# Kernel optimization log

Measured on AMD Instinct MI355X. Metric: run time of the kernel, lower is better.

## Reference

```python
import jax, jax.numpy as jnp
import numpy as np

N_HEAD = 8
D_HEAD = 64
D_MODEL = 512
CTX = 64
B = 2
Q_LEN = 2048
T = Q_LEN + CTX - 1


def setup_inputs() -> dict:
    key = jax.random.key(0)
    ks = jax.random.split(key, 7)
    HD = N_HEAD * D_HEAD
    return {
        "x": jax.random.normal(ks[0], (B, T, D_MODEL), jnp.float32),
        "r": jax.random.normal(ks[1], (CTX, D_MODEL), jnp.float32),
        "Wkv": jax.random.normal(ks[2], (D_MODEL, 2 * HD), jnp.float32) * 0.02,
        "Wq": jax.random.normal(ks[3], (D_MODEL, HD), jnp.float32) * 0.02,
        "bq": jax.random.normal(ks[4], (HD,), jnp.float32) * 0.02,
        "Wr": jax.random.normal(ks[5], (D_MODEL, HD), jnp.float32) * 0.02,
        "Wo": jax.random.normal(ks[6], (HD, D_MODEL), jnp.float32) * 0.02,
    }


def reference(x, r, Wkv, Wq, bq, Wr, Wo):
    Bb, Tt, _ = x.shape
    C = r.shape[0]
    H, Dh = N_HEAD, D_HEAD
    q_len = Tt - C + 1
    scale = Dh ** -0.5

    kv = x @ Wkv                                  # [B, T, 2*H*Dh]
    k_all = kv[..., : H * Dh].reshape(Bb, Tt, H, Dh)
    v_all = kv[..., H * Dh:].reshape(Bb, Tt, H, Dh)

    # sliding windows (torch unfold(1, ctx, 1) equivalent)
    idx = jnp.arange(q_len)[:, None] + jnp.arange(C)[None, :]   # [q, C]
    k_win = k_all[:, idx]                         # [B, q, C, H, Dh]
    v_win = v_all[:, idx]                         # [B, q, C, H, Dh]

    hq = (x[:, C - 1:] @ Wq + bq).reshape(Bb, q_len, H, Dh)     # [B, q, H, Dh]
    hr = (r @ Wr).reshape(C, H, Dh)                              # [C, H, Dh]

    # q . (k + r): split into content term + relative-position bias term
    scores = (jnp.einsum('bqhd,bqchd->bhqc', hq, k_win)
              + jnp.einsum('bqhd,chd->bhqc', hq, hr)) * scale    # [B, H, q, C]

    # padding mask: positions in first ctx-1 steps that are all-zero
    pad_mask = jnp.all(x[:, : C - 1] == 0, axis=-1)              # [B, C-1]
    full_mask = jnp.concatenate(
        [pad_mask, jnp.zeros((Bb, q_len), dtype=bool)], axis=1)  # [B, T]
    mask_win = full_mask[:, idx]                                 # [B, q, C]
    scores = jnp.where(mask_win[:, None], -jnp.inf, scores)

    w = jax.nn.softmax(scores, axis=-1)                          # [B, H, q, C]
    out = jnp.einsum('bhqc,bqchd->bqhd', w, v_win).reshape(Bb, q_len, H * Dh)
    return out @ Wo                                              # [B, q, d_model]
```

## Files before the change

kernel.cpp:

```cpp
#include <hip/hip_runtime.h>
#include <cstdint>
#include <cstddef>

#define NH 8
#define DH 64
#define DM 512
#define CTX 64
#define BB 2
#define QL 2048
#define TT (QL + CTX - 1)
#define HDIM 512
#define KVN 1024
#define KD 512

typedef unsigned short u16;
typedef __attribute__((ext_vector_type(8))) short bf16x8;
typedef __attribute__((ext_vector_type(4))) float f32x4;

__device__ __forceinline__ u16 f2bf(float f) {
    uint32_t u = __float_as_uint(f);
    u += 0x7FFF + ((u >> 16) & 1);
    return (u16)(u >> 16);
}
__device__ __forceinline__ uint32_t packbf(float lo, float hi) {
    return (uint32_t)f2bf(lo) | ((uint32_t)f2bf(hi) << 16);
}

#define GLLDS(g, l) __builtin_amdgcn_global_load_lds( \
    (const __attribute__((address_space(1))) void*)(g), \
    (__attribute__((address_space(3))) void*)(l), 16, 0, 0)

__global__ __launch_bounds__(256) void prep_kernel(
    const float* __restrict__ Wkv, const float* __restrict__ Wq,
    const float* __restrict__ Wr, const float* __restrict__ Wo,
    u16* __restrict__ WkvqT, u16* __restrict__ WrT, u16* __restrict__ WoT)
{
    __shared__ float tile[64][65];
    const int bid = blockIdx.x;
    const int tid = threadIdx.x;

    const float* W; u16* WT; int N; int tidx;
    if (bid < 128)      { W = Wkv; WT = WkvqT;                    N = 1024; tidx = bid; }
    else if (bid < 192) { W = Wq;  WT = WkvqT + (size_t)1024*512; N = 512;  tidx = bid - 128; }
    else if (bid < 256) { W = Wr;  WT = WrT;                      N = 512;  tidx = bid - 192; }
    else                { W = Wo;  WT = WoT;                      N = 512;  tidx = bid - 256; }
    const int tpr = N / 64;
    const int kb = (tidx / tpr) * 64, nb = (tidx % tpr) * 64;
    const int c4 = (tid & 15) * 4;
    for (int kk = tid >> 4; kk < 64; kk += 16) {
        float4 v = *(const float4*)&W[(size_t)(kb + kk) * N + nb + c4];
        tile[kk][c4 + 0] = v.x; tile[kk][c4 + 1] = v.y;
        tile[kk][c4 + 2] = v.z; tile[kk][c4 + 3] = v.w;
    }
    __syncthreads();
    for (int nn = tid >> 4; nn < 64; nn += 16) {
        ushort4 o;
        o.x = f2bf(tile[c4 + 0][nn]); o.y = f2bf(tile[c4 + 1][nn]);
        o.z = f2bf(tile[c4 + 2][nn]); o.w = f2bf(tile[c4 + 3][nn]);
        *(ushort4*)&WT[(size_t)(nb + nn) * KD + kb + c4] = o;
    }
}

__global__ __launch_bounds__(256) void gemm_fused(
    const float* __restrict__ x, const u16* __restrict__ WkvqT,
    u16* __restrict__ kvb, u16* __restrict__ hqb, const float* __restrict__ bq,
    const float* __restrict__ r, const u16* __restrict__ WrT,
    u16* __restrict__ hrb, float* __restrict__ maskv)
{
    const int bid = blockIdx.x;
    const int tid = threadIdx.x;

    if (bid >= 400) {
        __shared__ int anyflag;
        int idx = bid - 400;
        int t = idx >> 1, b = idx & 1;
        const float* row = x + (size_t)(b * TT + t) * DM;
        bool nz = (row[tid] != 0.f) || (row[tid + 256] != 0.f);
        if (tid == 0) anyflag = 0;
        __syncthreads();
        unsigned long long bal = __ballot(nz);
        if ((tid & 63) == 0 && bal) atomicOr(&anyflag, 1);
        __syncthreads();
        if (tid == 0) maskv[b * 64 + t] = anyflag ? 0.f : -1e30f;
        return;
    }

    __shared__ __align__(16) u16 As[2][128 * 32];
    __shared__ __align__(16) u16 Bs[2][128 * 32];

    const int lane = tid & 63;
    const int w    = tid >> 6;
    const int wm   = (w >> 1) * 64;
    const int wn   = (w & 1) * 64;

    const bool g3 = (bid >= 396);
    const float* A; const u16* BT; int m0, n0, mrows;
    if (g3) { A = r; BT = WrT;   m0 = 0;                n0 = (bid - 396) * 128; mrows = CTX; }
    else    { A = x; BT = WkvqT; m0 = (bid / 12) * 128; n0 = (bid % 12) * 128;  mrows = BB * TT; }

    const int arow = tid >> 1;
    const int akh  = (tid & 1) * 16;
    int grow = m0 + arow; if (grow >= mrows) grow = 0;
    const float* gA = A + (size_t)grow * KD + akh;

    const int am0 = tid >> 2;
    const int ak0 = (tid & 3) * 8;
    const u16* gb0 = BT + (size_t)(n0 + am0) * KD + ak0;
    const u16* gb1 = gb0 + (size_t)64 * KD;

    float4 f0, f1, f2, f3;
#define ALOAD(kt) do { \
    f0 = *(const float4*)(gA + (kt));      f1 = *(const float4*)(gA + (kt) + 4); \
    f2 = *(const float4*)(gA + (kt) + 8);  f3 = *(const float4*)(gA + (kt) + 12); \
} while (0)
#define AWRITE(buf) do { \
    uint4 p0, p1; \
    p0.x = packbf(f0.x, f0.y); p0.y = packbf(f0.z, f0.w); \
    p0.z = packbf(f1.x, f1.y); p0.w = packbf(f1.z, f1.w); \
    p1.x = packbf(f2.x, f2.y); p1.y = packbf(f2.z, f2.w); \
    p1.z = packbf(f3.x, f3.y); p1.w = packbf(f3.z, f3.w); \
    *(uint4*)&As[buf][arow * 32 + akh]     = p0; \
    *(uint4*)&As[buf][arow * 32 + akh + 8] = p1; \
} while (0)
#define BSTAGE(buf, kt) do { \
    GLLDS(gb0 + (kt), &Bs[buf][(size_t)w * 512]); \
    GLLDS(gb1 + (kt), &Bs[buf][2048 + (size_t)w * 512]); \
} while (0)

    f32x4 acc[4][4];
#pragma unroll
    for (int i = 0; i < 4; i++)
#pragma unroll
        for (int j = 0; j < 4; j++)
            acc[i][j] = (f32x4){0.f, 0.f, 0.f, 0.f};

    ALOAD(0);
    AWRITE(0);
    BSTAGE(0, 0);
    __syncthreads();

    int cur = 0;
    const int fm = lane & 15;
    const int fk = (lane >> 4) * 8;
    for (int kt = 0; kt < KD; kt += 32) {
        const bool more = (kt + 32 < KD);
        if (more) { ALOAD(kt + 32); BSTAGE(cur ^ 1, kt + 32); }

        bf16x8 af[4], bfr[4];
#pragma unroll
        for (int i = 0; i < 4; i++)
            af[i] = *(const bf16x8*)&As[cur][(wm + i * 16 + fm) * 32 + fk];
#pragma unroll
        for (int j = 0; j < 4; j++)
            bfr[j] = *(const bf16x8*)&Bs[cur][(wn + j * 16 + fm) * 32 + fk];
#pragma unroll
        for (int i = 0; i < 4; i++)
#pragma unroll
            for (int j = 0; j < 4; j++)
                acc[i][j] = __builtin_amdgcn_mfma_f32_16x16x32_bf16(af[i], bfr[j], acc[i][j], 0, 0, 0);

        if (more) AWRITE(cur ^ 1);
        __syncthreads();
        cur ^= 1;
    }
#undef ALOAD
#undef AWRITE
#undef BSTAGE

    const int fc = lane & 15;
    const int fr = (lane >> 4) * 4;
    if (!g3) {
        const bool iskv = (n0 < 1024);
#pragma unroll
        for (int i = 0; i < 4; i++)
#pragma unroll
            for (int rr = 0; rr < 4; rr++) {
                int row = m0 + wm + i * 16 + fr + rr;
                if (row < BB * TT) {
                    if (iskv) {
#pragma unroll
                        for (int j = 0; j < 4; j++) {
                            int col = n0 + wn + j * 16 + fc;
                            kvb[(size_t)row * KVN + col] = f2bf(acc[i][j][rr]);
                        }
                    } else {
                        int bb = row / TT;
                        int t  = row - bb * TT;
                        if (t >= CTX - 1) {
                            size_t orow = (size_t)(bb * QL + t - (CTX - 1));
#pragma unroll
                            for (int j = 0; j < 4; j++) {
                                int col = n0 + wn + j * 16 + fc - 1024;
                                hqb[orow * HDIM + col] = f2bf(acc[i][j][rr] + bq[col]);
                            }
                        }
                    }
                }
            }
    } else {
#pragma unroll
        for (int i = 0; i < 4; i++)
#pragma unroll
            for (int rr = 0; rr < 4; rr++) {
                int row = m0 + wm + i * 16 + fr + rr;
                if (row < CTX) {
#pragma unroll
                    for (int j = 0; j < 4; j++) {
                        int col = n0 + wn + j * 16 + fc;
                        hrb[(size_t)row * HDIM + col] = f2bf(acc[i][j][rr]);
                    }
                }
            }
    }
}

__global__ __launch_bounds__(256) void gemm_n64(
    const u16* __restrict__ A, const u16* __restrict__ BT,
    float* __restrict__ C, int M, int N)
{
    __shared__ u16 As[2][128 * 32];
    __shared__ u16 Bs[2][64 * 32];

    const int tid  = threadIdx.x;
    const int lane = tid & 63;
    const int w    = tid >> 6;
    const int wm   = (w >> 1) * 64;
    const int wn   = (w & 1) * 32;
    const int m0   = blockIdx.y * 128;
    const int n0   = blockIdx.x * 64;

    const int am0 = tid >> 2;
    const int ak0 = (tid & 3) * 8;
    const u16* ga0 = A  + (size_t)(m0 + am0) * KD + ak0;
    const u16* ga1 = ga0 + (size_t)64 * KD;
    const u16* gb0 = BT + (size_t)(n0 + am0) * KD + ak0;

#define STAGE_G2(buf, kt) do { \
    GLLDS(ga0 + (kt), &As[buf][(size_t)w * 512]); \
    GLLDS(ga1 + (kt), &As[buf][2048 + (size_t)w * 512]); \
    GLLDS(gb0 + (kt), &Bs[buf][(size_t)w * 512]); \
} while (0)

    f32x4 acc[4][2];
#pragma unroll
    for (int i = 0; i < 4; i++)
#pragma unroll
        for (int j = 0; j < 2; j++)
            acc[i][j] = (f32x4){0.f, 0.f, 0.f, 0.f};

    STAGE_G2(0, 0);
    __syncthreads();

    int cur = 0;
    const int fm = lane & 15;
    const int fk = (lane >> 4) * 8;
    for (int kt = 0; kt < KD; kt += 32) {
        if (kt + 32 < KD) STAGE_G2(cur ^ 1, kt + 32);

        bf16x8 af[4], bfr[2];
#pragma unroll
        for (int i = 0; i < 4; i++)
            af[i] = *(const bf16x8*)&As[cur][(wm + i * 16 + fm) * 32 + fk];
#pragma unroll
        for (int j = 0; j < 2; j++)
            bfr[j] = *(const bf16x8*)&Bs[cur][(wn + j * 16 + fm) * 32 + fk];
#pragma unroll
        for (int i = 0; i < 4; i++)
#pragma unroll
            for (int j = 0; j < 2; j++)
                acc[i][j] = __builtin_amdgcn_mfma_f32_16x16x32_bf16(af[i], bfr[j], acc[i][j], 0, 0, 0);

        __syncthreads();
        cur ^= 1;
    }
#undef STAGE_G2

    const int fc = lane & 15;
    const int fr = (lane >> 4) * 4;
#pragma unroll
    for (int i = 0; i < 4; i++)
#pragma unroll
        for (int rr = 0; rr < 4; rr++) {
            int row = m0 + wm + i * 16 + fr + rr;
            if (row < M) {
#pragma unroll
                for (int j = 0; j < 2; j++) {
                    int col = n0 + wn + j * 16 + fc;
                    C[(size_t)row * N + col] = acc[i][j][rr];
                }
            }
        }
}

__global__ __launch_bounds__(256) void attn_mfma(
    const u16* __restrict__ kvb, const u16* __restrict__ hqb,
    const u16* __restrict__ hrb, const float* __restrict__ maskv,
    u16* __restrict__ attnb)
{
    __shared__ __align__(16) char lds[55296];
    float* sprime = (float*)lds;
    u16*   vTs    = (u16*)(lds + 20480);
    u16*   wband  = (u16*)(lds + 37888);

    const int q0 = blockIdx.x * 64;
    const int h  = blockIdx.y;
    const int b  = blockIdx.z;
    const int tid  = threadIdx.x;
    const int lane = tid & 63;
    const int w    = tid >> 6;
    const int qb   = q0 + w * 16;

    const int vr0 = tid >> 4;
    const int vc4 = (tid & 15) * 4;
    ushort4 vreg[8];
#pragma unroll
    for (int i = 0; i < 8; i++) {
        int rr = vr0 + i * 16;
        if (rr < 127)
            vreg[i] = *(const ushort4*)&kvb[(size_t)(b * TT + q0 + rr) * KVN + HDIM + h * DH + vc4];
        else
            vreg[i] = (ushort4){0, 0, 0, 0};
    }

    {
        uint32_t* wz = (uint32_t*)wband;
#pragma unroll
        for (int i = 0; i < 17; i++) wz[tid + i * 256] = 0;
    }
    asm volatile("s_waitcnt lgkmcnt(0)" ::: "memory");
    __builtin_amdgcn_s_barrier();

    const int fm = lane & 15;
    const int fk = (lane >> 4) * 8;

    const u16* hqrow = hqb + (size_t)(b * QL + qb + fm) * HDIM + h * DH + fk;
    bf16x8 afr0 = *(const bf16x8*)(hqrow);
    bf16x8 afr1 = *(const bf16x8*)(hqrow + 32);

    {
        const u16* kbase = kvb + (size_t)(b * TT + qb + fm) * KVN + h * DH + fk;
#pragma unroll
        for (int nt = 0; nt < 5; nt++) {
            bf16x8 b0 = *(const bf16x8*)(kbase + (size_t)nt * 16 * KVN);
            bf16x8 b1 = *(const bf16x8*)(kbase + (size_t)nt * 16 * KVN + 32);
            f32x4 acc = (f32x4){0.f, 0.f, 0.f, 0.f};
            acc = __builtin_amdgcn_mfma_f32_16x16x32_bf16(afr0, b0, acc, 0, 0, 0);
            acc = __builtin_amdgcn_mfma_f32_16x16x32_bf16(afr1, b1, acc, 0, 0, 0);
            const int row = (lane >> 4) * 4;
#pragma unroll
            for (int r = 0; r < 4; r++)
                sprime[w * 1280 + (row + r) * 80 + nt * 16 + fm] = acc[r];
        }
    }
    {
        const u16* hrbase = hrb + (size_t)fm * HDIM + h * DH + fk;
#pragma unroll
        for (int nc = 0; nc < 4; nc++) {
            bf16x8 b0 = *(const bf16x8*)(hrbase + (size_t)nc * 16 * HDIM);
            bf16x8 b1 = *(const bf16x8*)(hrbase + (size_t)nc * 16 * HDIM + 32);
            f32x4 acc = (f32x4){0.f, 0.f, 0.f, 0.f};
            acc = __builtin_amdgcn_mfma_f32_16x16x32_bf16(afr0, b0, acc, 0, 0, 0);
            acc = __builtin_amdgcn_mfma_f32_16x16x32_bf16(afr1, b1, acc, 0, 0, 0);
            const int row = (lane >> 4) * 4;
#pragma unroll
            for (int r = 0; r < 4; r++)
                sprime[w * 1280 + (row + r) * 81 + nc * 16 + fm] += acc[r];
        }
    }

#pragma unroll
    for (int i = 0; i < 8; i++) {
        int rr = vr0 + i * 16;
        vTs[(vc4 + 0) * 136 + rr] = vreg[i].x;
        vTs[(vc4 + 1) * 136 + rr] = vreg[i].y;
        vTs[(vc4 + 2) * 136 + rr] = vreg[i].z;
        vTs[(vc4 + 3) * 136 + rr] = vreg[i].w;
    }

    {
        const int i  = lane >> 2;
        const int g  = lane & 3;
        const int qloc = w * 16 + i;
        const float* srow = &sprime[w * 1280 + i * 81 + g * 16];
        float sv[16];
#pragma unroll
        for (int j = 0; j < 16; j++) sv[j] = srow[j] * 0.125f;
        if (q0 == 0) {
#pragma unroll
            for (int j = 0; j < 16; j++) {
                int t = qloc + g * 16 + j;
                if (t < 63) sv[j] += maskv[b * 64 + t];
            }
        }
        float mx = sv[0];
#pragma unroll
        for (int j = 1; j < 16; j++) mx = fmaxf(mx, sv[j]);
        mx = fmaxf(mx, __shfl_xor(mx, 1, 64));
        mx = fmaxf(mx, __shfl_xor(mx, 2, 64));
        float sum = 0.f;
#pragma unroll
        for (int j = 0; j < 16; j++) { sv[j] = __expf(sv[j] - mx); sum += sv[j]; }
        sum += __shfl_xor(sum, 1, 64);
        sum += __shfl_xor(sum, 2, 64);
        float inv = 1.f / sum;
        u16* wrow = &wband[qloc * 136 + qloc + g * 16];
#pragma unroll
        for (int j = 0; j < 16; j++) wrow[j] = f2bf(sv[j] * inv);
    }
    __syncthreads();

    f32x4 oacc[4];
#pragma unroll
    for (int j = 0; j < 4; j++) oacc[j] = (f32x4){0.f, 0.f, 0.f, 0.f};
#pragma unroll
    for (int ks = 0; ks < 4; ks++) {
        bf16x8 wa = *(const bf16x8*)&wband[(w * 16 + fm) * 136 + ks * 32 + fk];
#pragma unroll
        for (int j = 0; j < 4; j++) {
            bf16x8 vb = *(const bf16x8*)&vTs[(j * 16 + fm) * 136 + ks * 32 + fk];
            oacc[j] = __builtin_amdgcn_mfma_f32_16x16x32_bf16(wa, vb, oacc[j], 0, 0, 0);
        }
    }
    {
        const int row = (lane >> 4) * 4;
#pragma unroll
        for (int j = 0; j < 4; j++)
#pragma unroll
            for (int r = 0; r < 4; r++)
                attnb[(size_t)(b * QL + qb + row + r) * HDIM + h * DH + j * 16 + fm] =
                    f2bf(oacc[j][r]);
    }
}

extern "C" void kernel_launch(void* const* d_in, const int* in_sizes, int n_in,
                              void* d_out, int out_size, void* d_ws, size_t ws_size,
                              hipStream_t stream)
{
    const float* x   = (const float*)d_in[0];
    const float* r   = (const float*)d_in[1];
    const float* Wkv = (const float*)d_in[2];
    const float* Wq  = (const float*)d_in[3];
    const float* bq  = (const float*)d_in[4];
    const float* Wr  = (const float*)d_in[5];
    const float* Wo  = (const float*)d_in[6];
    float* out = (float*)d_out;

    char* p = (char*)d_ws;
    u16* WkvqT  = (u16*)p;  p += (size_t)1536 * 512 * 2;
    u16* WrT    = (u16*)p;  p += (size_t)512 * 512 * 2;
    u16* WoT    = (u16*)p;  p += (size_t)512 * 512 * 2;
    u16* kvb    = (u16*)p;  p += (size_t)4224 * 1024 * 2;
    u16* hqb    = (u16*)p;  p += (size_t)4096 * 512 * 2;
    u16* hrb    = (u16*)p;  p += (size_t)64 * 512 * 2;
    u16* attnb  = (u16*)p;  p += (size_t)4096 * 512 * 2;
    float* maskv = (float*)p;

    hipLaunchKernelGGL(prep_kernel, dim3(320), dim3(256), 0, stream,
                       Wkv, Wq, Wr, Wo, WkvqT, WrT, WoT);
    hipLaunchKernelGGL(gemm_fused, dim3(528), dim3(256), 0, stream,
                       x, WkvqT, kvb, hqb, bq, r, WrT, hrb, maskv);
    hipLaunchKernelGGL(attn_mfma, dim3(QL / 64, NH, BB), dim3(256), 0, stream,
                       kvb, hqb, hrb, maskv, attnb);
    hipLaunchKernelGGL(gemm_n64, dim3(512 / 64, 4096 / 128), dim3(256), 0, stream,
                       attnb, WoT, out, 4096, 512);
}
```

Before: 125.4 us.

## Fuse all stages into one cooperative persistent kernel with grid syncs

Merges the weight-prep, QKV/R projection GEMM, attention and output GEMM kernels into a single cooperative kernel of 512 blocks that separates the stages with grid.sync, falling back to four separate launches if the cooperative launch fails. The mask computation moves from the projection GEMM into the prep stage. The output GEMM is retiled from 128x64 to 64x64 so its 512 tiles match the grid. The aim is to remove per-launch overhead and inter-kernel gaps. In exchange, the kernel carries the 55 KB LDS footprint of the attention stage everywhere, and the stages pay grid-barrier costs and run many idle blocks.

```diff
diff --git a/kernel.cpp b/kernel.cpp
--- a/kernel.cpp
+++ b/kernel.cpp
@@ -1,6 +1,9 @@
 #include <hip/hip_runtime.h>
+#include <hip/hip_cooperative_groups.h>
 #include <cstdint>
 #include <cstddef>
+
+namespace cg = cooperative_groups;
 
 #define NH 8
 #define DH 64
@@ -30,63 +33,60 @@
     (const __attribute__((address_space(1))) void*)(g), \
     (__attribute__((address_space(3))) void*)(l), 16, 0, 0)
 
-__global__ __launch_bounds__(256) void prep_kernel(
+__device__ __forceinline__ void st_prep(
+    char* lds, int bid, int tid,
+    const float* __restrict__ x,
     const float* __restrict__ Wkv, const float* __restrict__ Wq,
     const float* __restrict__ Wr, const float* __restrict__ Wo,
-    u16* __restrict__ WkvqT, u16* __restrict__ WrT, u16* __restrict__ WoT)
-{
-    __shared__ float tile[64][65];
-    const int bid = blockIdx.x;
-    const int tid = threadIdx.x;
-
-    const float* W; u16* WT; int N; int tidx;
-    if (bid < 128)      { W = Wkv; WT = WkvqT;                    N = 1024; tidx = bid; }
-    else if (bid < 192) { W = Wq;  WT = WkvqT + (size_t)1024*512; N = 512;  tidx = bid - 128; }
-    else if (bid < 256) { W = Wr;  WT = WrT;                      N = 512;  tidx = bid - 192; }
-    else                { W = Wo;  WT = WoT;                      N = 512;  tidx = bid - 256; }
-    const int tpr = N / 64;
-    const int kb = (tidx / tpr) * 64, nb = (tidx % tpr) * 64;
-    const int c4 = (tid & 15) * 4;
-    for (int kk = tid >> 4; kk < 64; kk += 16) {
-        float4 v = *(const float4*)&W[(size_t)(kb + kk) * N + nb + c4];
-        tile[kk][c4 + 0] = v.x; tile[kk][c4 + 1] = v.y;
-        tile[kk][c4 + 2] = v.z; tile[kk][c4 + 3] = v.w;
-    }
-    __syncthreads();
-    for (int nn = tid >> 4; nn < 64; nn += 16) {
-        ushort4 o;
-        o.x = f2bf(tile[c4 + 0][nn]); o.y = f2bf(tile[c4 + 1][nn]);
-        o.z = f2bf(tile[c4 + 2][nn]); o.w = f2bf(tile[c4 + 3][nn]);
-        *(ushort4*)&WT[(size_t)(nb + nn) * KD + kb + c4] = o;
-    }
-}
-
-__global__ __launch_bounds__(256) void gemm_fused(
+    u16* __restrict__ WkvqT, u16* __restrict__ WrT, u16* __restrict__ WoT,
+    float* __restrict__ maskv)
+{
+    if (bid < 320) {
+        float (*tile)[65] = (float (*)[65])lds;
+        const float* W; u16* WT; int N; int tidx;
+        if (bid < 128)      { W = Wkv; WT = WkvqT;                    N = 1024; tidx = bid; }
+        else if (bid < 192) { W = Wq;  WT = WkvqT + (size_t)1024*512; N = 512;  tidx = bid - 128; }
+        else if (bid < 256) { W = Wr;  WT = WrT;                      N = 512;  tidx = bid - 192; }
+        else                { W = Wo;  WT = WoT;                      N = 512;  tidx = bid - 256; }
+        const int tpr = N / 64;
+        const int kb = (tidx / tpr) * 64, nb = (tidx % tpr) * 64;
+        const int c4 = (tid & 15) * 4;
+        for (int kk = tid >> 4; kk < 64; kk += 16) {
+            float4 v = *(const float4*)&W[(size_t)(kb + kk) * N + nb + c4];
+            tile[kk][c4 + 0] = v.x; tile[kk][c4 + 1] = v.y;
+            tile[kk][c4 + 2] = v.z; tile[kk][c4 + 3] = v.w;
+        }
+        __syncthreads();
+        for (int nn = tid >> 4; nn < 64; nn += 16) {
+            ushort4 o;
+            o.x = f2bf(tile[c4 + 0][nn]); o.y = f2bf(tile[c4 + 1][nn]);
+            o.z = f2bf(tile[c4 + 2][nn]); o.w = f2bf(tile[c4 + 3][nn]);
+            *(ushort4*)&WT[(size_t)(nb + nn) * KD + kb + c4] = o;
+        }
+    } else {
+        int* anyflag = (int*)lds;
+        int idx = bid - 320;
+        int t = idx >> 1, b = idx & 1;
+        const float* row = x + (size_t)(b * TT + t) * DM;
+        bool nz = (row[tid] != 0.f) || (row[tid + 256] != 0.f);
+        if (tid == 0) *anyflag = 0;
+        __syncthreads();
+        unsigned long long bal = __ballot(nz);
+        if ((tid & 63) == 0 && bal) atomicOr(anyflag, 1);
+        __syncthreads();
+        if (tid == 0) maskv[b * 64 + t] = *anyflag ? 0.f : -1e30f;
+    }
+}
+
+__device__ __forceinline__ void st_g1(
+    char* lds, int bid, int tid,
     const float* __restrict__ x, const u16* __restrict__ WkvqT,
     u16* __restrict__ kvb, u16* __restrict__ hqb, const float* __restrict__ bq,
     const float* __restrict__ r, const u16* __restrict__ WrT,
-    u16* __restrict__ hrb, float* __restrict__ maskv)
-{
-    const int bid = blockIdx.x;
-    const int tid = threadIdx.x;
-
-    if (bid >= 400) {
-        __shared__ int anyflag;
-        int idx = bid - 400;
-        int t = idx >> 1, b = idx & 1;
-        const float* row = x + (size_t)(b * TT + t) * DM;
-        bool nz = (row[tid] != 0.f) || (row[tid + 256] != 0.f);
-        if (tid == 0) anyflag = 0;
-        __syncthreads();
-        unsigned long long bal = __ballot(nz);
-        if ((tid & 63) == 0 && bal) atomicOr(&anyflag, 1);
-        __syncthreads();
-        if (tid == 0) maskv[b * 64 + t] = anyflag ? 0.f : -1e30f;
-        return;
-    }
-
-    __shared__ __align__(16) u16 As[2][128 * 32];
-    __shared__ __align__(16) u16 Bs[2][128 * 32];
+    u16* __restrict__ hrb)
+{
+    u16 (*As)[128 * 32] = (u16 (*)[128 * 32])lds;
+    u16 (*Bs)[128 * 32] = (u16 (*)[128 * 32])(lds + 16384);
 
     const int lane = tid & 63;
     const int w    = tid >> 6;
@@ -109,11 +109,11 @@
     const u16* gb1 = gb0 + (size_t)64 * KD;
 
     float4 f0, f1, f2, f3;
-#define ALOAD(kt) do { \
+#define ALOAD1(kt) do { \
     f0 = *(const float4*)(gA + (kt));      f1 = *(const float4*)(gA + (kt) + 4); \
     f2 = *(const float4*)(gA + (kt) + 8);  f3 = *(const float4*)(gA + (kt) + 12); \
 } while (0)
-#define AWRITE(buf) do { \
+#define AWRITE1(buf) do { \
     uint4 p0, p1; \
     p0.x = packbf(f0.x, f0.y); p0.y = packbf(f0.z, f0.w); \
     p0.z = packbf(f1.x, f1.y); p0.w = packbf(f1.z, f1.w); \
@@ -122,7 +122,7 @@
     *(uint4*)&As[buf][arow * 32 + akh]     = p0; \
     *(uint4*)&As[buf][arow * 32 + akh + 8] = p1; \
 } while (0)
-#define BSTAGE(buf, kt) do { \
+#define BSTAGE1(buf, kt) do { \
     GLLDS(gb0 + (kt), &Bs[buf][(size_t)w * 512]); \
     GLLDS(gb1 + (kt), &Bs[buf][2048 + (size_t)w * 512]); \
 } while (0)
@@ -134,9 +134,9 @@
         for (int j = 0; j < 4; j++)
             acc[i][j] = (f32x4){0.f, 0.f, 0.f, 0.f};
 
-    ALOAD(0);
-    AWRITE(0);
-    BSTAGE(0, 0);
+    ALOAD1(0);
+    AWRITE1(0);
+    BSTAGE1(0, 0);
     __syncthreads();
 
     int cur = 0;
@@ -144,7 +144,7 @@
     const int fk = (lane >> 4) * 8;
     for (int kt = 0; kt < KD; kt += 32) {
         const bool more = (kt + 32 < KD);
-        if (more) { ALOAD(kt + 32); BSTAGE(cur ^ 1, kt + 32); }
+        if (more) { ALOAD1(kt + 32); BSTAGE1(cur ^ 1, kt + 32); }
 
         bf16x8 af[4], bfr[4];
 #pragma unroll
@@ -159,13 +159,13 @@
             for (int j = 0; j < 4; j++)
                 acc[i][j] = __builtin_amdgcn_mfma_f32_16x16x32_bf16(af[i], bfr[j], acc[i][j], 0, 0, 0);
 
-        if (more) AWRITE(cur ^ 1);
+        if (more) AWRITE1(cur ^ 1);
         __syncthreads();
         cur ^= 1;
     }
-#undef ALOAD
-#undef AWRITE
-#undef BSTAGE
+#undef ALOAD1
+#undef AWRITE1
+#undef BSTAGE1
 
     const int fc = lane & 15;
     const int fr = (lane >> 4) * 4;
@@ -214,98 +214,19 @@
     }
 }
 
-__global__ __launch_bounds__(256) void gemm_n64(
-    const u16* __restrict__ A, const u16* __restrict__ BT,
-    float* __restrict__ C, int M, int N)
-{
-    __shared__ u16 As[2][128 * 32];
-    __shared__ u16 Bs[2][64 * 32];
-
-    const int tid  = threadIdx.x;
-    const int lane = tid & 63;
-    const int w    = tid >> 6;
-    const int wm   = (w >> 1) * 64;
-    const int wn   = (w & 1) * 32;
-    const int m0   = blockIdx.y * 128;
-    const int n0   = blockIdx.x * 64;
-
-    const int am0 = tid >> 2;
-    const int ak0 = (tid & 3) * 8;
-    const u16* ga0 = A  + (size_t)(m0 + am0) * KD + ak0;
-    const u16* ga1 = ga0 + (size_t)64 * KD;
-    const u16* gb0 = BT + (size_t)(n0 + am0) * KD + ak0;
-
-#define STAGE_G2(buf, kt) do { \
-    GLLDS(ga0 + (kt), &As[buf][(size_t)w * 512]); \
-    GLLDS(ga1 + (kt), &As[buf][2048 + (size_t)w * 512]); \
-    GLLDS(gb0 + (kt), &Bs[buf][(size_t)w * 512]); \
-} while (0)
-
-    f32x4 acc[4][2];
-#pragma unroll
-    for (int i = 0; i < 4; i++)
-#pragma unroll
-        for (int j = 0; j < 2; j++)
-            acc[i][j] = (f32x4){0.f, 0.f, 0.f, 0.f};
-
-    STAGE_G2(0, 0);
-    __syncthreads();
-
-    int cur = 0;
-    const int fm = lane & 15;
-    const int fk = (lane >> 4) * 8;
-    for (int kt = 0; kt < KD; kt += 32) {
-        if (kt + 32 < KD) STAGE_G2(cur ^ 1, kt + 32);
-
-        bf16x8 af[4], bfr[2];
-#pragma unroll
-        for (int i = 0; i < 4; i++)
-            af[i] = *(const bf16x8*)&As[cur][(wm + i * 16 + fm) * 32 + fk];
-#pragma unroll
-        for (int j = 0; j < 2; j++)
-            bfr[j] = *(const bf16x8*)&Bs[cur][(wn + j * 16 + fm) * 32 + fk];
-#pragma unroll
-        for (int i = 0; i < 4; i++)
-#pragma unroll
-            for (int j = 0; j < 2; j++)
-                acc[i][j] = __builtin_amdgcn_mfma_f32_16x16x32_bf16(af[i], bfr[j], acc[i][j], 0, 0, 0);
-
-        __syncthreads();
-        cur ^= 1;
-    }
-#undef STAGE_G2
-
-    const int fc = lane & 15;
-    const int fr = (lane >> 4) * 4;
-#pragma unroll
-    for (int i = 0; i < 4; i++)
-#pragma unroll
-        for (int rr = 0; rr < 4; rr++) {
-            int row = m0 + wm + i * 16 + fr + rr;
-            if (row < M) {
-#pragma unroll
-                for (int j = 0; j < 2; j++) {
-                    int col = n0 + wn + j * 16 + fc;
-                    C[(size_t)row * N + col] = acc[i][j][rr];
-                }
-            }
-        }
-}
-
-__global__ __launch_bounds__(256) void attn_mfma(
+__device__ __forceinline__ void st_attn(
+    char* lds, int bid, int tid,
     const u16* __restrict__ kvb, const u16* __restrict__ hqb,
     const u16* __restrict__ hrb, const float* __restrict__ maskv,
     u16* __restrict__ attnb)
 {
-    __shared__ __align__(16) char lds[55296];
     float* sprime = (float*)lds;
     u16*   vTs    = (u16*)(lds + 20480);
     u16*   wband  = (u16*)(lds + 37888);
 
-    const int q0 = blockIdx.x * 64;
-    const int h  = blockIdx.y;
-    const int b  = blockIdx.z;
-    const int tid  = threadIdx.x;
+    const int q0 = (bid & 31) * 64;
+    const int h  = (bid >> 5) & 7;
+    const int b  = bid >> 8;
     const int lane = tid & 63;
     const int w    = tid >> 6;
     const int qb   = q0 + w * 16;
@@ -348,8 +269,8 @@
             acc = __builtin_amdgcn_mfma_f32_16x16x32_bf16(afr1, b1, acc, 0, 0, 0);
             const int row = (lane >> 4) * 4;
 #pragma unroll
-            for (int r = 0; r < 4; r++)
-                sprime[w * 1280 + (row + r) * 80 + nt * 16 + fm] = acc[r];
+            for (int r2 = 0; r2 < 4; r2++)
+                sprime[w * 1280 + (row + r2) * 80 + nt * 16 + fm] = acc[r2];
         }
     }
     {
@@ -363,8 +284,8 @@
             acc = __builtin_amdgcn_mfma_f32_16x16x32_bf16(afr1, b1, acc, 0, 0, 0);
             const int row = (lane >> 4) * 4;
 #pragma unroll
-            for (int r = 0; r < 4; r++)
-                sprime[w * 1280 + (row + r) * 81 + nc * 16 + fm] += acc[r];
+            for (int r2 = 0; r2 < 4; r2++)
+                sprime[w * 1280 + (row + r2) * 81 + nc * 16 + fm] += acc[r2];
         }
     }
 
@@ -426,10 +347,149 @@
 #pragma unroll
         for (int j = 0; j < 4; j++)
 #pragma unroll
-            for (int r = 0; r < 4; r++)
-                attnb[(size_t)(b * QL + qb + row + r) * HDIM + h * DH + j * 16 + fm] =
-                    f2bf(oacc[j][r]);
-    }
+            for (int r2 = 0; r2 < 4; r2++)
+                attnb[(size_t)(b * QL + qb + row + r2) * HDIM + h * DH + j * 16 + fm] =
+                    f2bf(oacc[j][r2]);
+    }
+}
+
+__device__ __forceinline__ void st_g2(
+    char* lds, int bid, int tid,
+    const u16* __restrict__ A, const u16* __restrict__ BT,
+    float* __restrict__ C)
+{
+    u16 (*As)[64 * 32] = (u16 (*)[64 * 32])lds;
+    u16 (*Bs)[64 * 32] = (u16 (*)[64 * 32])(lds + 8192);
+
+    const int lane = tid & 63;
+    const int w    = tid >> 6;
+    const int wm   = (w >> 1) * 32;
+    const int wn   = (w & 1) * 32;
+    const int m0   = (bid >> 3) * 64;
+    const int n0   = (bid & 7) * 64;
+
+    const int am0 = tid >> 2;
+    const int ak0 = (tid & 3) * 8;
+    const u16* ga0 = A  + (size_t)(m0 + am0) * KD + ak0;
+    const u16* gb0 = BT + (size_t)(n0 + am0) * KD + ak0;
+
+    f32x4 acc[2][2];
+#pragma unroll
+    for (int i = 0; i < 2; i++)
+#pragma unroll
+        for (int j = 0; j < 2; j++)
+            acc[i][j] = (f32x4){0.f, 0.f, 0.f, 0.f};
+
+    GLLDS(ga0, &As[0][(size_t)w * 512]);
+    GLLDS(gb0, &Bs[0][(size_t)w * 512]);
+    __syncthreads();
+
+    int cur = 0;
+    const int fm = lane & 15;
+    const int fk = (lane >> 4) * 8;
+    for (int kt = 0; kt < KD; kt += 32) {
+        if (kt + 32 < KD) {
+            GLLDS(ga0 + kt + 32, &As[cur ^ 1][(size_t)w * 512]);
+            GLLDS(gb0 + kt + 32, &Bs[cur ^ 1][(size_t)w * 512]);
+        }
+        bf16x8 af[2], bfr[2];
+#pragma unroll
+        for (int i = 0; i < 2; i++)
+            af[i] = *(const bf16x8*)&As[cur][(wm + i * 16 + fm) * 32 + fk];
+#pragma unroll
+        for (int j = 0; j < 2; j++)
+            bfr[j] = *(const bf16x8*)&Bs[cur][(wn + j * 16 + fm) * 32 + fk];
+#pragma unroll
+        for (int i = 0; i < 2; i++)
+#pragma unroll
+            for (int j = 0; j < 2; j++)
+                acc[i][j] = __builtin_amdgcn_mfma_f32_16x16x32_bf16(af[i], bfr[j], acc[i][j], 0, 0, 0);
+        __syncthreads();
+        cur ^= 1;
+    }
+
+    const int fc = lane & 15;
+    const int fr = (lane >> 4) * 4;
+#pragma unroll
+    for (int i = 0; i < 2; i++)
+#pragma unroll
+        for (int rr = 0; rr < 2 * 2; rr++)
+            ;
+#pragma unroll
+    for (int i = 0; i < 2; i++)
+#pragma unroll
+        for (int rr = 0; rr < 4; rr++) {
+            int row = m0 + wm + i * 16 + fr + rr;
+#pragma unroll
+            for (int j = 0; j < 2; j++) {
+                int col = n0 + wn + j * 16 + fc;
+                C[(size_t)row * HDIM + col] = acc[i][j][rr];
+            }
+        }
+}
+
+__global__ __launch_bounds__(256, 2) void mega(
+    const float* __restrict__ x, const float* __restrict__ r,
+    const float* __restrict__ Wkv, const float* __restrict__ Wq,
+    const float* __restrict__ bq, const float* __restrict__ Wr,
+    const float* __restrict__ Wo, float* __restrict__ out,
+    u16* __restrict__ WkvqT, u16* __restrict__ WrT, u16* __restrict__ WoT,
+    u16* __restrict__ kvb, u16* __restrict__ hqb, u16* __restrict__ hrb,
+    u16* __restrict__ attnb, float* __restrict__ maskv)
+{
+    __shared__ __align__(16) char lds[55296];
+    cg::grid_group grid = cg::this_grid();
+    const int bid = blockIdx.x;
+    const int tid = threadIdx.x;
+
+    if (bid < 448) st_prep(lds, bid, tid, x, Wkv, Wq, Wr, Wo, WkvqT, WrT, WoT, maskv);
+    __threadfence();
+    grid.sync();
+
+    if (bid < 400) st_g1(lds, bid, tid, x, WkvqT, kvb, hqb, bq, r, WrT, hrb);
+    __threadfence();
+    grid.sync();
+
+    st_attn(lds, bid, tid, kvb, hqb, hrb, maskv, attnb);
+    __threadfence();
+    grid.sync();
+
+    st_g2(lds, bid, tid, attnb, WoT, out);
+}
+
+__global__ __launch_bounds__(256) void k_prep(
+    const float* __restrict__ x,
+    const float* __restrict__ Wkv, const float* __restrict__ Wq,
+    const float* __restrict__ Wr, const float* __restrict__ Wo,
+    u16* __restrict__ WkvqT, u16* __restrict__ WrT, u16* __restrict__ WoT,
+    float* __restrict__ maskv)
+{
+    __shared__ __align__(16) char lds[16640];
+    st_prep(lds, blockIdx.x, threadIdx.x, x, Wkv, Wq, Wr, Wo, WkvqT, WrT, WoT, maskv);
+}
+__global__ __launch_bounds__(256) void k_g1(
+    const float* __restrict__ x, const u16* __restrict__ WkvqT,
+    u16* __restrict__ kvb, u16* __restrict__ hqb, const float* __restrict__ bq,
+    const float* __restrict__ r, const u16* __restrict__ WrT,
+    u16* __restrict__ hrb)
+{
+    __shared__ __align__(16) char lds[32768];
+    st_g1(lds, blockIdx.x, threadIdx.x, x, WkvqT, kvb, hqb, bq, r, WrT, hrb);
+}
+__global__ __launch_bounds__(256) void k_attn(
+    const u16* __restrict__ kvb, const u16* __restrict__ hqb,
+    const u16* __restrict__ hrb, const float* __restrict__ maskv,
+    u16* __restrict__ attnb)
+{
+    __shared__ __align__(16) char lds[55296];
+    st_attn(lds, blockIdx.x, threadIdx.x, kvb, hqb, hrb, maskv, attnb);
+}
+__global__ __launch_bounds__(256) void k_g2(
+    const u16* __restrict__ attnb, const u16* __restrict__ WoT,
+    float* __restrict__ out)
+{
+    __shared__ __align__(16) char lds[16384];
+    st_g2(lds, blockIdx.x, threadIdx.x, attnb, WoT, out);
 }
 
 extern "C" void kernel_launch(void* const* d_in, const int* in_sizes, int n_in,
@@ -455,12 +515,22 @@
     u16* attnb  = (u16*)p;  p += (size_t)4096 * 512 * 2;
     float* maskv = (float*)p;
 
-    hipLaunchKernelGGL(prep_kernel, dim3(320), dim3(256), 0, stream,
-                       Wkv, Wq, Wr, Wo, WkvqT, WrT, WoT);
-    hipLaunchKernelGGL(gemm_fused, dim3(528), dim3(256), 0, stream,
-                       x, WkvqT, kvb, hqb, bq, r, WrT, hrb, maskv);
-    hipLaunchKernelGGL(attn_mfma, dim3(QL / 64, NH, BB), dim3(256), 0, stream,
-                       kvb, hqb, hrb, maskv, attnb);
-    hipLaunchKernelGGL(gemm_n64, dim3(512 / 64, 4096 / 128), dim3(256), 0, stream,
-                       attnb, WoT, out, 4096, 512);
-}
+    void* args[16] = {
+        (void*)&x, (void*)&r, (void*)&Wkv, (void*)&Wq, (void*)&bq,
+        (void*)&Wr, (void*)&Wo, (void*)&out, (void*)&WkvqT, (void*)&WrT,
+        (void*)&WoT, (void*)&kvb, (void*)&hqb, (void*)&hrb, (void*)&attnb,
+        (void*)&maskv };
+
+    hipError_t e = hipLaunchCooperativeKernel((const void*)mega, dim3(512), dim3(256),
+                                              (void**)args, 0, stream);
+    if (e != hipSuccess) {
+        hipLaunchKernelGGL(k_prep, dim3(448), dim3(256), 0, stream,
+                           x, Wkv, Wq, Wr, Wo, WkvqT, WrT, WoT, maskv);
+        hipLaunchKernelGGL(k_g1, dim3(400), dim3(256), 0, stream,
+                           x, WkvqT, kvb, hqb, bq, r, WrT, hrb);
+        hipLaunchKernelGGL(k_attn, dim3(512), dim3(256), 0, stream,
+                           kvb, hqb, hrb, maskv, attnb);
+        hipLaunchKernelGGL(k_g2, dim3(512), dim3(256), 0, stream,
+                           attnb, WoT, out);
+    }
+}
```

New measurement: 478.2 us. +281.2%, slower.

## Shrink GEMM tiles for more blocks and alias attention LDS buffers

Applied to the files above, without the earlier changes.

The fused projection GEMM now uses 128x64 tiles instead of 128x128, doubling its grid to 928 blocks. The output projection GEMM uses 64x64 tiles with 512 blocks. In the attention kernel, the softmax is moved ahead of the V transpose so the V buffer can share LDS with the score buffer, cutting LDS use from 54KB to 37KB and adding a launch bound of 4 blocks per SM. The goal is better CU fill and occupancy, at the cost of less data reuse per tile and an extra barrier-ordered reuse of LDS.

```diff
diff --git a/kernel.cpp b/kernel.cpp
--- a/kernel.cpp
+++ b/kernel.cpp
@@ -70,9 +70,9 @@
     const int bid = blockIdx.x;
     const int tid = threadIdx.x;
 
-    if (bid >= 400) {
+    if (bid >= 800) {
         __shared__ int anyflag;
-        int idx = bid - 400;
+        int idx = bid - 800;
         int t = idx >> 1, b = idx & 1;
         const float* row = x + (size_t)(b * TT + t) * DM;
         bool nz = (row[tid] != 0.f) || (row[tid + 256] != 0.f);
@@ -86,34 +86,32 @@
     }
 
     __shared__ __align__(16) u16 As[2][128 * 32];
-    __shared__ __align__(16) u16 Bs[2][128 * 32];
+    __shared__ __align__(16) u16 Bs[2][64 * 32];
 
     const int lane = tid & 63;
     const int w    = tid >> 6;
-    const int wm   = (w >> 1) * 64;
-    const int wn   = (w & 1) * 64;
-
-    const bool g3 = (bid >= 396);
+    const int wm   = w * 32;
+
+    const bool g3 = (bid >= 792);
     const float* A; const u16* BT; int m0, n0, mrows;
-    if (g3) { A = r; BT = WrT;   m0 = 0;                n0 = (bid - 396) * 128; mrows = CTX; }
-    else    { A = x; BT = WkvqT; m0 = (bid / 12) * 128; n0 = (bid % 12) * 128;  mrows = BB * TT; }
+    if (g3) { A = r; BT = WrT;   m0 = 0;                n0 = (bid - 792) * 64; mrows = CTX; }
+    else    { A = x; BT = WkvqT; m0 = (bid / 24) * 128; n0 = (bid % 24) * 64;  mrows = BB * TT; }
 
     const int arow = tid >> 1;
     const int akh  = (tid & 1) * 16;
     int grow = m0 + arow; if (grow >= mrows) grow = 0;
     const float* gA = A + (size_t)grow * KD + akh;
 
-    const int am0 = tid >> 2;
-    const int ak0 = (tid & 3) * 8;
-    const u16* gb0 = BT + (size_t)(n0 + am0) * KD + ak0;
-    const u16* gb1 = gb0 + (size_t)64 * KD;
+    const int bn0 = tid >> 2;
+    const int bk0 = (tid & 3) * 8;
+    const u16* gb0 = BT + (size_t)(n0 + bn0) * KD + bk0;
 
     float4 f0, f1, f2, f3;
-#define ALOAD(kt) do { \
+#define ALOAD1(kt) do { \
     f0 = *(const float4*)(gA + (kt));      f1 = *(const float4*)(gA + (kt) + 4); \
     f2 = *(const float4*)(gA + (kt) + 8);  f3 = *(const float4*)(gA + (kt) + 12); \
 } while (0)
-#define AWRITE(buf) do { \
+#define AWRITE1(buf) do { \
     uint4 p0, p1; \
     p0.x = packbf(f0.x, f0.y); p0.y = packbf(f0.z, f0.w); \
     p0.z = packbf(f1.x, f1.y); p0.w = packbf(f1.z, f1.w); \
@@ -122,21 +120,18 @@
     *(uint4*)&As[buf][arow * 32 + akh]     = p0; \
     *(uint4*)&As[buf][arow * 32 + akh + 8] = p1; \
 } while (0)
-#define BSTAGE(buf, kt) do { \
-    GLLDS(gb0 + (kt), &Bs[buf][(size_t)w * 512]); \
-    GLLDS(gb1 + (kt), &Bs[buf][2048 + (size_t)w * 512]); \
-} while (0)
-
-    f32x4 acc[4][4];
-#pragma unroll
-    for (int i = 0; i < 4; i++)
+#define BSTAGE1(buf, kt) GLLDS(gb0 + (kt), &Bs[buf][(size_t)w * 512])
+
+    f32x4 acc[2][4];
+#pragma unroll
+    for (int i = 0; i < 2; i++)
 #pragma unroll
         for (int j = 0; j < 4; j++)
             acc[i][j] = (f32x4){0.f, 0.f, 0.f, 0.f};
 
-    ALOAD(0);
-    AWRITE(0);
-    BSTAGE(0, 0);
+    ALOAD1(0);
+    AWRITE1(0);
+    BSTAGE1(0, 0);
     __syncthreads();
 
     int cur = 0;
@@ -144,35 +139,35 @@
     const int fk = (lane >> 4) * 8;
     for (int kt = 0; kt < KD; kt += 32) {
         const bool more = (kt + 32 < KD);
-        if (more) { ALOAD(kt + 32); BSTAGE(cur ^ 1, kt + 32); }
-
-        bf16x8 af[4], bfr[4];
-#pragma unroll
-        for (int i = 0; i < 4; i++)
+        if (more) { ALOAD1(kt + 32); BSTAGE1(cur ^ 1, kt + 32); }
+
+        bf16x8 af[2], bfr[4];
+#pragma unroll
+        for (int i = 0; i < 2; i++)
             af[i] = *(const bf16x8*)&As[cur][(wm + i * 16 + fm) * 32 + fk];
 #pragma unroll
         for (int j = 0; j < 4; j++)
-            bfr[j] = *(const bf16x8*)&Bs[cur][(wn + j * 16 + fm) * 32 + fk];
-#pragma unroll
-        for (int i = 0; i < 4; i++)
+            bfr[j] = *(const bf16x8*)&Bs[cur][(j * 16 + fm) * 32 + fk];
+#pragma unroll
+        for (int i = 0; i < 2; i++)
 #pragma unroll
             for (int j = 0; j < 4; j++)
                 acc[i][j] = __builtin_amdgcn_mfma_f32_16x16x32_bf16(af[i], bfr[j], acc[i][j], 0, 0, 0);
 
-        if (more) AWRITE(cur ^ 1);
+        if (more) AWRITE1(cur ^ 1);
         __syncthreads();
         cur ^= 1;
     }
-#undef ALOAD
-#undef AWRITE
-#undef BSTAGE
+#undef ALOAD1
+#undef AWRITE1
+#undef BSTAGE1
 
     const int fc = lane & 15;
     const int fr = (lane >> 4) * 4;
     if (!g3) {
         const bool iskv = (n0 < 1024);
 #pragma unroll
-        for (int i = 0; i < 4; i++)
+        for (int i = 0; i < 2; i++)
 #pragma unroll
             for (int rr = 0; rr < 4; rr++) {
                 int row = m0 + wm + i * 16 + fr + rr;
@@ -180,7 +175,7 @@
                     if (iskv) {
 #pragma unroll
                         for (int j = 0; j < 4; j++) {
-                            int col = n0 + wn + j * 16 + fc;
+                            int col = n0 + j * 16 + fc;
                             kvb[(size_t)row * KVN + col] = f2bf(acc[i][j][rr]);
                         }
                     } else {
@@ -190,7 +185,7 @@
                             size_t orow = (size_t)(bb * QL + t - (CTX - 1));
 #pragma unroll
                             for (int j = 0; j < 4; j++) {
-                                int col = n0 + wn + j * 16 + fc - 1024;
+                                int col = n0 + j * 16 + fc - 1024;
                                 hqb[orow * HDIM + col] = f2bf(acc[i][j][rr] + bq[col]);
                             }
                         }
@@ -199,14 +194,14 @@
             }
     } else {
 #pragma unroll
-        for (int i = 0; i < 4; i++)
+        for (int i = 0; i < 2; i++)
 #pragma unroll
             for (int rr = 0; rr < 4; rr++) {
                 int row = m0 + wm + i * 16 + fr + rr;
                 if (row < CTX) {
 #pragma unroll
                     for (int j = 0; j < 4; j++) {
-                        int col = n0 + wn + j * 16 + fc;
+                        int col = n0 + j * 16 + fc;
                         hrb[(size_t)row * HDIM + col] = f2bf(acc[i][j][rr]);
                     }
                 }
@@ -214,93 +209,15 @@
     }
 }
 
-__global__ __launch_bounds__(256) void gemm_n64(
-    const u16* __restrict__ A, const u16* __restrict__ BT,
-    float* __restrict__ C, int M, int N)
-{
-    __shared__ u16 As[2][128 * 32];
-    __shared__ u16 Bs[2][64 * 32];
-
-    const int tid  = threadIdx.x;
-    const int lane = tid & 63;
-    const int w    = tid >> 6;
-    const int wm   = (w >> 1) * 64;
-    const int wn   = (w & 1) * 32;
-    const int m0   = blockIdx.y * 128;
-    const int n0   = blockIdx.x * 64;
-
-    const int am0 = tid >> 2;
-    const int ak0 = (tid & 3) * 8;
-    const u16* ga0 = A  + (size_t)(m0 + am0) * KD + ak0;
-    const u16* ga1 = ga0 + (size_t)64 * KD;
-    const u16* gb0 = BT + (size_t)(n0 + am0) * KD + ak0;
-
-#define STAGE_G2(buf, kt) do { \
-    GLLDS(ga0 + (kt), &As[buf][(size_t)w * 512]); \
-    GLLDS(ga1 + (kt), &As[buf][2048 + (size_t)w * 512]); \
-    GLLDS(gb0 + (kt), &Bs[buf][(size_t)w * 512]); \
-} while (0)
-
-    f32x4 acc[4][2];
-#pragma unroll
-    for (int i = 0; i < 4; i++)
-#pragma unroll
-        for (int j = 0; j < 2; j++)
-            acc[i][j] = (f32x4){0.f, 0.f, 0.f, 0.f};
-
-    STAGE_G2(0, 0);
-    __syncthreads();
-
-    int cur = 0;
-    const int fm = lane & 15;
-    const int fk = (lane >> 4) * 8;
-    for (int kt = 0; kt < KD; kt += 32) {
-        if (kt + 32 < KD) STAGE_G2(cur ^ 1, kt + 32);
-
-        bf16x8 af[4], bfr[2];
-#pragma unroll
-        for (int i = 0; i < 4; i++)
-            af[i] = *(const bf16x8*)&As[cur][(wm + i * 16 + fm) * 32 + fk];
-#pragma unroll
-        for (int j = 0; j < 2; j++)
-            bfr[j] = *(const bf16x8*)&Bs[cur][(wn + j * 16 + fm) * 32 + fk];
-#pragma unroll
-        for (int i = 0; i < 4; i++)
-#pragma unroll
-            for (int j = 0; j < 2; j++)
-                acc[i][j] = __builtin_amdgcn_mfma_f32_16x16x32_bf16(af[i], bfr[j], acc[i][j], 0, 0, 0);
-
-        __syncthreads();
-        cur ^= 1;
-    }
-#undef STAGE_G2
-
-    const int fc = lane & 15;
-    const int fr = (lane >> 4) * 4;
-#pragma unroll
-    for (int i = 0; i < 4; i++)
-#pragma unroll
-        for (int rr = 0; rr < 4; rr++) {
-            int row = m0 + wm + i * 16 + fr + rr;
-            if (row < M) {
-#pragma unroll
-                for (int j = 0; j < 2; j++) {
-                    int col = n0 + wn + j * 16 + fc;
-                    C[(size_t)row * N + col] = acc[i][j][rr];
-                }
-            }
-        }
-}
-
-__global__ __launch_bounds__(256) void attn_mfma(
+__global__ __launch_bounds__(256, 4) void attn_mfma(
     const u16* __restrict__ kvb, const u16* __restrict__ hqb,
     const u16* __restrict__ hrb, const float* __restrict__ maskv,
     u16* __restrict__ attnb)
 {
-    __shared__ __align__(16) char lds[55296];
+    __shared__ __align__(16) char lds[37888];
     float* sprime = (float*)lds;
-    u16*   vTs    = (u16*)(lds + 20480);
-    u16*   wband  = (u16*)(lds + 37888);
+    u16*   vTs    = (u16*)lds;
+    u16*   wband  = (u16*)(lds + 20480);
 
     const int q0 = blockIdx.x * 64;
     const int h  = blockIdx.y;
@@ -348,8 +265,8 @@
             acc = __builtin_amdgcn_mfma_f32_16x16x32_bf16(afr1, b1, acc, 0, 0, 0);
             const int row = (lane >> 4) * 4;
 #pragma unroll
-            for (int r = 0; r < 4; r++)
-                sprime[w * 1280 + (row + r) * 80 + nt * 16 + fm] = acc[r];
+            for (int r2 = 0; r2 < 4; r2++)
+                sprime[w * 1280 + (row + r2) * 80 + nt * 16 + fm] = acc[r2];
         }
     }
     {
@@ -363,10 +280,42 @@
             acc = __builtin_amdgcn_mfma_f32_16x16x32_bf16(afr1, b1, acc, 0, 0, 0);
             const int row = (lane >> 4) * 4;
 #pragma unroll
-            for (int r = 0; r < 4; r++)
-                sprime[w * 1280 + (row + r) * 81 + nc * 16 + fm] += acc[r];
-        }
-    }
+            for (int r2 = 0; r2 < 4; r2++)
+                sprime[w * 1280 + (row + r2) * 81 + nc * 16 + fm] += acc[r2];
+        }
+    }
+
+    {
+        const int i  = lane >> 2;
+        const int g  = lane & 3;
+        const int qloc = w * 16 + i;
+        const float* srow = &sprime[w * 1280 + i * 81 + g * 16];
+        float sv[16];
+#pragma unroll
+        for (int j = 0; j < 16; j++) sv[j] = srow[j] * 0.125f;
+        if (q0 == 0) {
+#pragma unroll
+            for (int j = 0; j < 16; j++) {
+                int t = qloc + g * 16 + j;
+                if (t < 63) sv[j] += maskv[b * 64 + t];
+            }
+        }
+        float mx = sv[0];
+#pragma unroll
+        for (int j = 1; j < 16; j++) mx = fmaxf(mx, sv[j]);
+        mx = fmaxf(mx, __shfl_xor(mx, 1, 64));
+        mx = fmaxf(mx, __shfl_xor(mx, 2, 64));
+        float sum = 0.f;
+#pragma unroll
+        for (int j = 0; j < 16; j++) { sv[j] = __expf(sv[j] - mx); sum += sv[j]; }
+        sum += __shfl_xor(sum, 1, 64);
+        sum += __shfl_xor(sum, 2, 64);
+        float inv = 1.f / sum;
+        u16* wrow = &wband[qloc * 136 + qloc + g * 16];
+#pragma unroll
+        for (int j = 0; j < 16; j++) wrow[j] = f2bf(sv[j] * inv);
+    }
+    __syncthreads();
 
 #pragma unroll
     for (int i = 0; i < 8; i++) {
@@ -376,37 +325,6 @@
         vTs[(vc4 + 2) * 136 + rr] = vreg[i].z;
         vTs[(vc4 + 3) * 136 + rr] = vreg[i].w;
     }
-
-    {
-        const int i  = lane >> 2;
-        const int g  = lane & 3;
-        const int qloc = w * 16 + i;
-        const float* srow = &sprime[w * 1280 + i * 81 + g * 16];
-        float sv[16];
-#pragma unroll
-        for (int j = 0; j < 16; j++) sv[j] = srow[j] * 0.125f;
-        if (q0 == 0) {
-#pragma unroll
-            for (int j = 0; j < 16; j++) {
-                int t = qloc + g * 16 + j;
-                if (t < 63) sv[j] += maskv[b * 64 + t];
-            }
-        }
-        float mx = sv[0];
-#pragma unroll
-        for (int j = 1; j < 16; j++) mx = fmaxf(mx, sv[j]);
-        mx = fmaxf(mx, __shfl_xor(mx, 1, 64));
-        mx = fmaxf(mx, __shfl_xor(mx, 2, 64));
-        float sum = 0.f;
-#pragma unroll
-        for (int j = 0; j < 16; j++) { sv[j] = __expf(sv[j] - mx); sum += sv[j]; }
-        sum += __shfl_xor(sum, 1, 64);
-        sum += __shfl_xor(sum, 2, 64);
-        float inv = 1.f / sum;
-        u16* wrow = &wband[qloc * 136 + qloc + g * 16];
-#pragma unroll
-        for (int j = 0; j < 16; j++) wrow[j] = f2bf(sv[j] * inv);
-    }
     __syncthreads();
 
     f32x4 oacc[4];
@@ -426,10 +344,80 @@
 #pragma unroll
         for (int j = 0; j < 4; j++)
 #pragma unroll
-            for (int r = 0; r < 4; r++)
-                attnb[(size_t)(b * QL + qb + row + r) * HDIM + h * DH + j * 16 + fm] =
-                    f2bf(oacc[j][r]);
-    }
+            for (int r2 = 0; r2 < 4; r2++)
+                attnb[(size_t)(b * QL + qb + row + r2) * HDIM + h * DH + j * 16 + fm] =
+                    f2bf(oacc[j][r2]);
+    }
+}
+
+__global__ __launch_bounds__(256) void gemm_n64(
+    const u16* __restrict__ A, const u16* __restrict__ BT,
+    float* __restrict__ C)
+{
+    __shared__ u16 As[2][64 * 32];
+    __shared__ u16 Bs[2][64 * 32];
+
+    const int tid  = threadIdx.x;
+    const int lane = tid & 63;
+    const int w    = tid >> 6;
+    const int wm   = (w >> 1) * 32;
+    const int wn   = (w & 1) * 32;
+    const int m0   = (blockIdx.x >> 3) * 64;
+    const int n0   = (blockIdx.x & 7) * 64;
+
+    const int am0 = tid >> 2;
+    const int ak0 = (tid & 3) * 8;
+    const u16* ga0 = A  + (size_t)(m0 + am0) * KD + ak0;
+    const u16* gb0 = BT + (size_t)(n0 + am0) * KD + ak0;
+
+    f32x4 acc[2][2];
+#pragma unroll
+    for (int i = 0; i < 2; i++)
+#pragma unroll
+        for (int j = 0; j < 2; j++)
+            acc[i][j] = (f32x4){0.f, 0.f, 0.f, 0.f};
+
+    GLLDS(ga0, &As[0][(size_t)w * 512]);
+    GLLDS(gb0, &Bs[0][(size_t)w * 512]);
+    __syncthreads();
+
+    int cur = 0;
+    const int fm = lane & 15;
+    const int fk = (lane >> 4) * 8;
+    for (int kt = 0; kt < KD; kt += 32) {
+        if (kt + 32 < KD) {
+            GLLDS(ga0 + kt + 32, &As[cur ^ 1][(size_t)w * 512]);
+            GLLDS(gb0 + kt + 32, &Bs[cur ^ 1][(size_t)w * 512]);
+        }
+        bf16x8 af[2], bfr[2];
+#pragma unroll
+        for (int i = 0; i < 2; i++)
+            af[i] = *(const bf16x8*)&As[cur][(wm + i * 16 + fm) * 32 + fk];
+#pragma unroll
+        for (int j = 0; j < 2; j++)
+            bfr[j] = *(const bf16x8*)&Bs[cur][(wn + j * 16 + fm) * 32 + fk];
+#pragma unroll
+        for (int i = 0; i < 2; i++)
+#pragma unroll
+            for (int j = 0; j < 2; j++)
+                acc[i][j] = __builtin_amdgcn_mfma_f32_16x16x32_bf16(af[i], bfr[j], acc[i][j], 0, 0, 0);
+        __syncthreads();
+        cur ^= 1;
+    }
+
+    const int fc = lane & 15;
+    const int fr = (lane >> 4) * 4;
+#pragma unroll
+    for (int i = 0; i < 2; i++)
+#pragma unroll
+        for (int rr = 0; rr < 4; rr++) {
+            int row = m0 + wm + i * 16 + fr + rr;
+#pragma unroll
+            for (int j = 0; j < 2; j++) {
+                int col = n0 + wn + j * 16 + fc;
+                C[(size_t)row * HDIM + col] = acc[i][j][rr];
+            }
+        }
 }
 
 extern "C" void kernel_launch(void* const* d_in, const int* in_sizes, int n_in,
@@ -457,10 +445,10 @@
 
     hipLaunchKernelGGL(prep_kernel, dim3(320), dim3(256), 0, stream,
                        Wkv, Wq, Wr, Wo, WkvqT, WrT, WoT);
-    hipLaunchKernelGGL(gemm_fused, dim3(528), dim3(256), 0, stream,
+    hipLaunchKernelGGL(gemm_fused, dim3(928), dim3(256), 0, stream,
                        x, WkvqT, kvb, hqb, bq, r, WrT, hrb, maskv);
     hipLaunchKernelGGL(attn_mfma, dim3(QL / 64, NH, BB), dim3(256), 0, stream,
                        kvb, hqb, hrb, maskv, attnb);
-    hipLaunchKernelGGL(gemm_n64, dim3(512 / 64, 4096 / 128), dim3(256), 0, stream,
-                       attnb, WoT, out, 4096, 512);
-}
+    hipLaunchKernelGGL(gemm_n64, dim3(512), dim3(256), 0, stream,
+                       attnb, WoT, out);
+}
```

Measured after the change: 125.4 us. About the same (+0.0%).
